# Kernel tuning notes

Hardware: AMD Instinct MI355X
Metric: run time of the kernel (lower is better)

Reference implementation:

```python
import jax, jax.numpy as jnp
import numpy as np

BS, C, H, W = 8, 64, 128, 128
KS = 3
SCALE = 2


def _pose_map(src_h, src_w, scale):
    # Vectorized version of positionKPN.pose_map (bilinear source coords).
    dst_h, dst_w = int(np.floor(src_h * scale)), int(np.floor(src_w * scale))
    scale_x, scale_y = float(src_w) / dst_w, float(src_h) / dst_h
    src_x = (np.arange(dst_w) + 0.5) * scale_x - 0.5
    src_y = (np.arange(dst_h) + 0.5) * scale_y - 0.5
    x0, y0 = np.floor(src_x), np.floor(src_y)
    inter_x = np.broadcast_to((x0 + 1).astype(np.int32)[None, :], (dst_h, dst_w))
    inter_y = np.broadcast_to((y0 + 1).astype(np.int32)[:, None], (dst_h, dst_w))
    fx = np.broadcast_to((src_x - x0).astype(np.float32)[None, :], (dst_h, dst_w))
    fy = np.broadcast_to((src_y - y0).astype(np.float32)[:, None], (dst_h, dst_w))
    pose = np.stack([fx, fy], axis=0).astype(np.float32)  # [2, dst_h, dst_w]
    return pose, np.ascontiguousarray(inter_y), np.ascontiguousarray(inter_x)


def setup_inputs() -> dict:
    key = jax.random.key(0)
    ks = jax.random.split(key, 8)
    pose, inter_y, inter_x = _pose_map(H, W, SCALE)
    s = 0.05
    return {
        "x": jax.random.normal(ks[0], (BS, C, H, W), dtype=jnp.float32),
        "scale": SCALE,
        "poseMap": jnp.asarray(pose),
        "interMapY": jnp.asarray(inter_y),
        "interMapX": jnp.asarray(inter_x),
        "W1": jax.random.normal(ks[1], (128, 2), dtype=jnp.float32) * s,
        "b1": jnp.zeros((128,), dtype=jnp.float32),
        "W2": jax.random.normal(ks[2], (256, 128), dtype=jnp.float32) * s,
        "b2": jnp.zeros((256,), dtype=jnp.float32),
        "W3": jax.random.normal(ks[3], (C * KS * KS, 256), dtype=jnp.float32) * s,
        "b3": jnp.zeros((C * KS * KS,), dtype=jnp.float32),
    }


def reference(x, scale, poseMap, interMapY, interMapX, W1, b1, W2, b2, W3, b3):
    bs, cs, h, w = x.shape
    ho, wo = interMapY.shape
    k2 = KS * KS
    # 1x1-conv MLP on position map -> per-pixel dynamic kernels.
    h1 = jax.nn.relu(jnp.einsum('oc,chw->ohw', W1, poseMap) + b1[:, None, None])
    h2 = jax.nn.relu(jnp.einsum('oc,chw->ohw', W2, h1) + b2[:, None, None])
    wgt = jnp.einsum('oc,chw->ohw', W3, h2) + b3[:, None, None]  # [cs*k2, ho, wo]
    wgt = wgt.reshape(cs, k2, ho, wo)
    # 3x3 patches gathered at source-grid centers interMap in [0, h] x [0, w]
    # (patch center y needs rows y-1..y+1 of x -> pad 1 before, 2 after).
    pad = KS // 2
    xp = jnp.pad(x, ((0, 0), (0, 0), (pad, pad + 1), (pad, pad + 1)))
    ky, kx = jnp.meshgrid(jnp.arange(KS), jnp.arange(KS), indexing='ij')
    Y = interMapY[None, :, :] + ky.reshape(k2, 1, 1)  # [k2, ho, wo]
    X = interMapX[None, :, :] + kx.reshape(k2, 1, 1)
    taps = xp[:, :, Y, X]  # [bs, cs, k2, ho, wo]
    out = jnp.einsum('bckyx,ckyx->bcyx', taps, wgt)  # per-pixel dynamic depthwise conv
    return out
```

## Files before the change

kernel.cpp:

```cpp
#include <hip/hip_runtime.h>

#define H_IN   128
#define W_IN   128
#define H_OUT  256
#define W_OUT  256
#define C_CH   64
#define B_SZ   8

__device__ __forceinline__ float rfl(float v) {
    return __uint_as_float(__builtin_amdgcn_readfirstlane(__float_as_uint(v)));
}

__global__ __launch_bounds__(576) void kpn_mlp(
    const float* __restrict__ pose,
    const float* __restrict__ W1,
    const float* __restrict__ b1,
    const float* __restrict__ W2,
    const float* __restrict__ b2,
    const float* __restrict__ W3,
    const float* __restrict__ b3,
    float* __restrict__ wgt4)
{
    __shared__ float h1[128];
    __shared__ float h2[256];

    const int p  = blockIdx.x;
    const int py = p >> 1, px = p & 1;
    const int t  = threadIdx.x;

    const float fx = pose[0 * H_OUT * W_OUT + py * W_OUT + px];
    const float fy = pose[1 * H_OUT * W_OUT + py * W_OUT + px];

    if (t < 128) {
        float a = W1[t * 2 + 0] * fx + W1[t * 2 + 1] * fy + b1[t];
        h1[t] = a > 0.f ? a : 0.f;
    }
    __syncthreads();

    if (t < 256) {
        float acc = b2[t];
        const float4* w = (const float4*)(W2 + t * 128);
        #pragma unroll 8
        for (int k = 0; k < 32; ++k) {
            float4 wv = w[k];
            acc += wv.x * h1[4 * k + 0] + wv.y * h1[4 * k + 1]
                 + wv.z * h1[4 * k + 2] + wv.w * h1[4 * k + 3];
        }
        h2[t] = acc > 0.f ? acc : 0.f;
    }
    __syncthreads();

    {
        float acc = b3[t];
        const float4* w = (const float4*)(W3 + t * 256);
        #pragma unroll 16
        for (int k = 0; k < 64; ++k) {
            float4 wv = w[k];
            acc += wv.x * h2[4 * k + 0] + wv.y * h2[4 * k + 1]
                 + wv.z * h2[4 * k + 2] + wv.w * h2[4 * k + 3];
        }
        const int c = t / 9, k = t - c * 9;
        wgt4[c * 48 + p * 12 + k] = acc;
    }
}

__global__ __launch_bounds__(256) void kpn_apply(
    const float* __restrict__ x,
    const float* __restrict__ wgt4,
    float* __restrict__ out)
{
    const int tx = threadIdx.x;
    const int ty = threadIdx.y;
    const int i  = blockIdx.x * 8 + ty;
    const int bc = blockIdx.y;
    const int c  = bc & 63;

    float w[4][9];
    const float* wp = wgt4 + c * 48;
    #pragma unroll
    for (int p = 0; p < 4; ++p) {
        float4 a = *(const float4*)(wp + p * 12);
        float4 b = *(const float4*)(wp + p * 12 + 4);
        float  g = wp[p * 12 + 8];
        w[p][0] = rfl(a.x); w[p][1] = rfl(a.y); w[p][2] = rfl(a.z); w[p][3] = rfl(a.w);
        w[p][4] = rfl(b.x); w[p][5] = rfl(b.y); w[p][6] = rfl(b.z); w[p][7] = rfl(b.w);
        w[p][8] = rfl(g);
    }

    const float* xp = x + (size_t)bc * (H_IN * W_IN);
    float t[4][7];
    #pragma unroll
    for (int r = 0; r < 4; ++r) {
        const int rr = i - 1 + r;
        if ((unsigned)rr < (unsigned)H_IN) {
            const float* rp = xp + rr * W_IN;
            float4 A = *(const float4*)(rp + 4 * tx);
            float2 B;
            if (tx < 31) B = *(const float2*)(rp + 4 * tx + 4);
            else         B = make_float2(0.f, 0.f);
            float m = __shfl_up(A.w, 1, 64);
            if (tx == 0) m = 0.f;
            t[r][0] = m;   t[r][1] = A.x; t[r][2] = A.y; t[r][3] = A.z;
            t[r][4] = A.w; t[r][5] = B.x; t[r][6] = B.y;
        } else {
            #pragma unroll
            for (int k2 = 0; k2 < 7; ++k2) t[r][k2] = 0.f;
        }
    }

    float o0[8], o1[8];
    #pragma unroll
    for (int k2 = 0; k2 < 8; ++k2) { o0[k2] = 0.f; o1[k2] = 0.f; }

    #pragma unroll
    for (int q = 0; q < 4; ++q) {
        #pragma unroll
        for (int ky = 0; ky < 3; ++ky) {
            #pragma unroll
            for (int kx = 0; kx < 3; ++kx) {
                const int k = ky * 3 + kx;
                o0[2*q    ] += t[ky    ][q + kx    ] * w[0][k];
                o0[2*q + 1] += t[ky    ][q + kx + 1] * w[1][k];
                o1[2*q    ] += t[ky + 1][q + kx    ] * w[2][k];
                o1[2*q + 1] += t[ky + 1][q + kx + 1] * w[3][k];
            }
        }
    }

    float* op = out + ((size_t)bc * H_OUT + 2 * i) * W_OUT + 8 * tx;
    *(float4*)(op)             = make_float4(o0[0], o0[1], o0[2], o0[3]);
    *(float4*)(op + 4)         = make_float4(o0[4], o0[5], o0[6], o0[7]);
    *(float4*)(op + W_OUT)     = make_float4(o1[0], o1[1], o1[2], o1[3]);
    *(float4*)(op + W_OUT + 4) = make_float4(o1[4], o1[5], o1[6], o1[7]);
}

extern "C" void kernel_launch(void* const* d_in, const int* in_sizes, int n_in,
                              void* d_out, int out_size, void* d_ws, size_t ws_size,
                              hipStream_t stream) {
    const float* x      = (const float*)d_in[0];
    const float* pose   = (const float*)d_in[2];
    const float* W1     = (const float*)d_in[5];
    const float* b1     = (const float*)d_in[6];
    const float* W2     = (const float*)d_in[7];
    const float* b2     = (const float*)d_in[8];
    const float* W3     = (const float*)d_in[9];
    const float* b3     = (const float*)d_in[10];
    float*       out    = (float*)d_out;
    float*       wgt4   = (float*)d_ws;

    kpn_mlp<<<dim3(4), dim3(576), 0, stream>>>(pose, W1, b1, W2, b2, W3, b3, wgt4);
    kpn_apply<<<dim3(16, 512), dim3(32, 8), 0, stream>>>(x, wgt4, out);
}
```

Baseline: 60.18 us.

## Stream 8 input rows per wave with rolling row buffer in kpn_apply

The apply kernel now has each wavefront of 64 lanes cover a full 128-wide input row with float2 loads, then march down 8 input rows while keeping a rolling 4-row register window. Each loaded row is reused across the output rows that need it, and horizontal neighbours come from shuffles. This is meant to cut the redundant reloading of 4 input rows per output row pair and to improve lane utilisation (64 lanes instead of 32 per row). The cost is fewer blocks (4x512 instead of 16x512), longer serial work per thread, and narrower per-thread stores.

```diff
diff --git a/kernel.cpp b/kernel.cpp
--- a/kernel.cpp
+++ b/kernel.cpp
@@ -69,69 +69,68 @@
     const float* __restrict__ wgt4,
     float* __restrict__ out)
 {
-    const int tx = threadIdx.x;
-    const int ty = threadIdx.y;
-    const int i  = blockIdx.x * 8 + ty;
+    const int l  = threadIdx.x;
+    const int wv = threadIdx.y;
     const int bc = blockIdx.y;
     const int c  = bc & 63;
+    const int i0 = blockIdx.x * 32 + wv * 8;
 
-    float w[4][9];
+    float wt[4][9];
     const float* wp = wgt4 + c * 48;
     #pragma unroll
     for (int p = 0; p < 4; ++p) {
-        float4 a = *(const float4*)(wp + p * 12);
-        float4 b = *(const float4*)(wp + p * 12 + 4);
-        float  g = wp[p * 12 + 8];
-        w[p][0] = rfl(a.x); w[p][1] = rfl(a.y); w[p][2] = rfl(a.z); w[p][3] = rfl(a.w);
-        w[p][4] = rfl(b.x); w[p][5] = rfl(b.y); w[p][6] = rfl(b.z); w[p][7] = rfl(b.w);
-        w[p][8] = rfl(g);
+        #pragma unroll
+        for (int k = 0; k < 9; ++k) wt[p][k] = rfl(wp[p * 12 + k]);
     }
 
-    const float* xp = x + (size_t)bc * (H_IN * W_IN);
-    float t[4][7];
-    #pragma unroll
-    for (int r = 0; r < 4; ++r) {
-        const int rr = i - 1 + r;
-        if ((unsigned)rr < (unsigned)H_IN) {
-            const float* rp = xp + rr * W_IN;
-            float4 A = *(const float4*)(rp + 4 * tx);
-            float2 B;
-            if (tx < 31) B = *(const float2*)(rp + 4 * tx + 4);
-            else         B = make_float2(0.f, 0.f);
-            float m = __shfl_up(A.w, 1, 64);
-            if (tx == 0) m = 0.f;
-            t[r][0] = m;   t[r][1] = A.x; t[r][2] = A.y; t[r][3] = A.z;
-            t[r][4] = A.w; t[r][5] = B.x; t[r][6] = B.y;
-        } else {
-            #pragma unroll
-            for (int k2 = 0; k2 < 7; ++k2) t[r][k2] = 0.f;
-        }
-    }
+    const float* xp = x + (size_t)bc * (H_IN * W_IN) + 2 * l;
 
-    float o0[8], o1[8];
-    #pragma unroll
-    for (int k2 = 0; k2 < 8; ++k2) { o0[k2] = 0.f; o1[k2] = 0.f; }
+    float M[4], A[4], B[4], D[4], E[4];
+
+    auto ldrow = [&](int rr, int s) {
+        float2 v = make_float2(0.f, 0.f);
+        if ((unsigned)rr < (unsigned)H_IN)
+            v = *(const float2*)(xp + rr * W_IN);
+        float m = __shfl_up(v.y, 1, 64);   if (l == 0)  m = 0.f;
+        float d = __shfl_down(v.x, 1, 64); if (l == 63) d = 0.f;
+        float e = __shfl_down(v.y, 1, 64); if (l == 63) e = 0.f;
+        M[s] = m; A[s] = v.x; B[s] = v.y; D[s] = d; E[s] = e;
+    };
+
+    ldrow(i0 - 1, 0);
+    ldrow(i0,     1);
+    ldrow(i0 + 1, 2);
+
+    float* op = out + ((size_t)bc * H_OUT + 2 * (size_t)i0) * W_OUT + 4 * l;
 
     #pragma unroll
-    for (int q = 0; q < 4; ++q) {
+    for (int q = 0; q < 8; ++q) {
+        ldrow(i0 + q + 2, (q + 3) & 3);
+        const int ss[4] = { q & 3, (q + 1) & 3, (q + 2) & 3, (q + 3) & 3 };
+
+        float ox0 = 0.f, ox1 = 0.f, ox2 = 0.f, ox3 = 0.f;
+        float oy0 = 0.f, oy1 = 0.f, oy2 = 0.f, oy3 = 0.f;
         #pragma unroll
         for (int ky = 0; ky < 3; ++ky) {
-            #pragma unroll
-            for (int kx = 0; kx < 3; ++kx) {
-                const int k = ky * 3 + kx;
-                o0[2*q    ] += t[ky    ][q + kx    ] * w[0][k];
-                o0[2*q + 1] += t[ky    ][q + kx + 1] * w[1][k];
-                o1[2*q    ] += t[ky + 1][q + kx    ] * w[2][k];
-                o1[2*q + 1] += t[ky + 1][q + kx + 1] * w[3][k];
-            }
+            const int su = ss[ky];
+            const int sl = ss[ky + 1];
+            const float w0a = wt[0][3*ky+0], w0b = wt[0][3*ky+1], w0c = wt[0][3*ky+2];
+            const float w1a = wt[1][3*ky+0], w1b = wt[1][3*ky+1], w1c = wt[1][3*ky+2];
+            const float w2a = wt[2][3*ky+0], w2b = wt[2][3*ky+1], w2c = wt[2][3*ky+2];
+            const float w3a = wt[3][3*ky+0], w3b = wt[3][3*ky+1], w3c = wt[3][3*ky+2];
+            ox0 += w0a * M[su] + w0b * A[su] + w0c * B[su];
+            ox1 += w1a * A[su] + w1b * B[su] + w1c * D[su];
+            ox2 += w0a * A[su] + w0b * B[su] + w0c * D[su];
+            ox3 += w1a * B[su] + w1b * D[su] + w1c * E[su];
+            oy0 += w2a * M[sl] + w2b * A[sl] + w2c * B[sl];
+            oy1 += w3a * A[sl] + w3b * B[sl] + w3c * D[sl];
+            oy2 += w2a * A[sl] + w2b * B[sl] + w2c * D[sl];
+            oy3 += w3a * B[sl] + w3b * D[sl] + w3c * E[sl];
         }
+        *(float4*)(op)         = make_float4(ox0, ox1, ox2, ox3);
+        *(float4*)(op + W_OUT) = make_float4(oy0, oy1, oy2, oy3);
+        op += 2 * W_OUT;
     }
-
-    float* op = out + ((size_t)bc * H_OUT + 2 * i) * W_OUT + 8 * tx;
-    *(float4*)(op)             = make_float4(o0[0], o0[1], o0[2], o0[3]);
-    *(float4*)(op + 4)         = make_float4(o0[4], o0[5], o0[6], o0[7]);
-    *(float4*)(op + W_OUT)     = make_float4(o1[0], o1[1], o1[2], o1[3]);
-    *(float4*)(op + W_OUT + 4) = make_float4(o1[4], o1[5], o1[6], o1[7]);
 }
 
 extern "C" void kernel_launch(void* const* d_in, const int* in_sizes, int n_in,
@@ -149,5 +148,5 @@
     float*       wgt4   = (float*)d_ws;
 
     kpn_mlp<<<dim3(4), dim3(576), 0, stream>>>(pose, W1, b1, W2, b2, W3, b3, wgt4);
-    kpn_apply<<<dim3(16, 512), dim3(32, 8), 0, stream>>>(x, wgt4, out);
+    kpn_apply<<<dim3(4, 512), dim3(64, 4), 0, stream>>>(x, wgt4, out);
 }
```

Result: faster. 56.02 us (-6.9%).
